# Optimization experiments

Hardware: AMD Instinct MI355X
Metric: run time of the kernel (lower is better)

## Reference

```python
import jax, jax.numpy as jnp
import numpy as np

NUM_HEADS = 8

def setup_inputs() -> dict:
    key = jax.random.key(0)
    k1, k2, k3 = jax.random.split(key, 3)
    B, N, C = 4, 4096, 512
    x = jax.random.normal(k1, (B, N, C), dtype=jnp.float32)
    w_qkv = jax.random.normal(k2, (C, 3 * C), dtype=jnp.float32) * (1.0 / np.sqrt(C))
    w_proj = jax.random.normal(k3, (C, C), dtype=jnp.float32) * (1.0 / np.sqrt(C))
    b_proj = jnp.zeros((C,), dtype=jnp.float32)
    return {"x": x, "w_qkv": w_qkv, "w_proj": w_proj, "b_proj": b_proj}

def reference(x, w_qkv, w_proj, b_proj):
    B, N, C = x.shape
    H = NUM_HEADS
    D = C // H
    # qkv projection (no bias), split into q, k, v of shape [B, H, N, D]
    qkv = (x @ w_qkv).reshape(B, N, 3, H, D)
    qkv = jnp.transpose(qkv, (2, 0, 3, 1, 4))
    q, k, v = qkv[0], qkv[1], qkv[2]
    # q: softmax over head_dim; k: elu(k)+1 then softmax over sequence dim
    q = jax.nn.softmax(q, axis=-1)
    k = jax.nn.softmax(jax.nn.elu(k) + 1.0, axis=-2)
    # linear attention: context = k^T @ v  -> [B, H, D, D]
    context = jnp.einsum('bhnd,bhne->bhde', k, v)
    # out = q @ context -> [B, H, N, D]
    out = jnp.einsum('bhnd,bhde->bhne', q, context)
    out = jnp.transpose(out, (0, 2, 1, 3)).reshape(B, N, C)
    # output projection (dropout with p=0.0 is identity)
    return out @ w_proj + b_proj
```

## Files before the change

kernel.cpp:

```cpp
#include <hip/hip_runtime.h>
#include <hip/hip_bf16.h>

typedef unsigned short u16;
typedef __attribute__((ext_vector_type(8))) short bhalf8;
typedef __attribute__((ext_vector_type(4))) float fx4;

struct __align__(8) US4 { u16 v[4]; };

__device__ __forceinline__ u16 f2bf(float x) {
  union { float f; unsigned int u; } c; c.f = x;
  unsigned int r = c.u + 0x7FFFu + ((c.u >> 16) & 1u);
  return (u16)(r >> 16);
}

__device__ __forceinline__ void gload16(const void* g, void* l) {
  __builtin_amdgcn_global_load_lds((const __attribute__((address_space(1))) void*)g,
                                   (__attribute__((address_space(3))) void*)l,
                                   16, 0, 0);
}

#define MFMA16(a, b, c) __builtin_amdgcn_mfma_f32_16x16x32_bf16((a), (b), (c), 0, 0, 0)

__global__ void k_conv(const float* __restrict__ in, u16* __restrict__ out, int n4) {
  int i = blockIdx.x * 256 + threadIdx.x;
  if (i < n4) {
    float4 v = ((const float4*)in)[i];
    US4 o;
    o.v[0] = f2bf(v.x); o.v[1] = f2bf(v.y); o.v[2] = f2bf(v.z); o.v[3] = f2bf(v.w);
    ((US4*)out)[i] = o;
  }
}

__global__ void k_transpose(const float* __restrict__ in, u16* __restrict__ out,
                            int R, int C, int rtiles, int remap) {
  __shared__ float tile[64][65];
  const int bx = blockIdx.x;
  const int rt = bx % rtiles, ct = bx / rtiles;
  const int r0 = rt * 64, c0 = ct * 64;
  const int t = threadIdx.x;
  #pragma unroll
  for (int i = 0; i < 16; ++i) {
    int e = i * 256 + t;
    int rr = e >> 6, cc = e & 63;
    tile[rr][cc] = in[(r0 + rr) * C + c0 + cc];
  }
  __syncthreads();
  #pragma unroll
  for (int i = 0; i < 16; ++i) {
    int e = i * 256 + t;
    int rr = e >> 6, cc = e & 63;
    int orow = c0 + rr;
    if (remap && orow >= 512) {
      int region = (orow - 512) >> 9;
      int within = (orow - 512) & 511;
      int h = within >> 6;
      orow = 512 + h * 128 + region * 64 + (within & 63);
    }
    out[orow * R + r0 + cc] = f2bf(tile[cc][rr]);
  }
}

__device__ __forceinline__ void gemm_core(const char* Ab, const char* Bb,
                                          char* As, char* Bs, fx4 acc[4][4]) {
  const int t = threadIdx.x;
  const int w = t >> 6, l = t & 63;
  const int wm = w >> 1, wn = w & 1;
  #pragma unroll 1
  for (int kt = 0; kt < 8; ++kt) {
    __syncthreads();
    const int kb = kt * 128;
    #pragma unroll
    for (int j = 0; j < 4; ++j) {
      int off = ((j * 4 + w) * 64 + l) * 16;
      int row = off >> 7;
      int colb = off & 127;
      int scol = colb ^ ((row & 7) << 4);
      gload16(Ab + row * 1024 + kb + scol, As + off);
      gload16(Bb + row * 1024 + kb + scol, Bs + off);
    }
    asm volatile("s_waitcnt vmcnt(0)" ::: "memory");
    __syncthreads();
    #pragma unroll
    for (int ks = 0; ks < 2; ++ks) {
      bhalf8 af[4], bfv[4];
      const int kbyte = ks * 64 + ((l >> 4) * 16);
      #pragma unroll
      for (int f = 0; f < 4; ++f) {
        int ra = wm * 64 + f * 16 + (l & 15);
        af[f] = *(const bhalf8*)(As + ra * 128 + (kbyte ^ ((ra & 7) << 4)));
        int rb = wn * 64 + f * 16 + (l & 15);
        bfv[f] = *(const bhalf8*)(Bs + rb * 128 + (kbyte ^ ((rb & 7) << 4)));
      }
      #pragma unroll
      for (int fm = 0; fm < 4; ++fm)
        #pragma unroll
        for (int fn = 0; fn < 4; ++fn)
          acc[fm][fn] = MFMA16(af[fm], bfv[fn], acc[fm][fn]);
    }
  }
}

__global__ __launch_bounds__(256, 2)
void k_qkv_gemm(const char* __restrict__ xb, const char* __restrict__ wqT,
                u16* __restrict__ qhat, float* __restrict__ ctx_part,
                float* __restrict__ z_part) {
  __shared__ __align__(16) char lds[32768];
  const int bx = blockIdx.x;
  const int tM = bx & 127, tN = bx >> 7;
  fx4 acc[4][4];
  const fx4 z4 = {0.f, 0.f, 0.f, 0.f};
  #pragma unroll
  for (int i = 0; i < 4; ++i)
    #pragma unroll
    for (int j = 0; j < 4; ++j) acc[i][j] = z4;

  gemm_core(xb + tM * 131072, wqT + tN * 131072, lds, lds + 16384, acc);

  const int t = threadIdx.x, w = t >> 6, l = t & 63;
  const int wm = w >> 1, wn = w & 1;
  const int m0 = tM * 128 + wm * 64;
  const int c0 = tN * 128 + wn * 64;

  if (tN < 4) {
    #pragma unroll
    for (int fm = 0; fm < 4; ++fm) {
      #pragma unroll
      for (int fn = 0; fn < 4; ++fn)
        #pragma unroll
        for (int r = 0; r < 4; ++r)
          acc[fm][fn][r] = __expf(acc[fm][fn][r]);
      fx4 s = acc[fm][0] + acc[fm][1] + acc[fm][2] + acc[fm][3];
      fx4 inv;
      #pragma unroll
      for (int r = 0; r < 4; ++r) {
        float sv = s[r];
        sv += __shfl_xor(sv, 1, 64);
        sv += __shfl_xor(sv, 2, 64);
        sv += __shfl_xor(sv, 4, 64);
        sv += __shfl_xor(sv, 8, 64);
        inv[r] = 1.0f / sv;
      }
      #pragma unroll
      for (int fn = 0; fn < 4; ++fn)
        #pragma unroll
        for (int r = 0; r < 4; ++r) {
          int m = m0 + fm * 16 + ((l >> 4) * 4) + r;
          int c = c0 + fn * 16 + (l & 15);
          qhat[m * 512 + c] = f2bf(acc[fm][fn][r] * inv[r]);
        }
    }
  } else {
    const int h = tN - 4;
    const int b = tM >> 5;
    const int mt = tM & 31;
    const int bh = b * 8 + h;
    char* ktb = lds;
    char* vtb = lds + 16384;
    __syncthreads();
    {
      char* dstb = (wn == 0) ? ktb : vtb;
      const bool isK = (wn == 0);
      #pragma unroll
      for (int fm = 0; fm < 4; ++fm)
        #pragma unroll
        for (int fn = 0; fn < 4; ++fn) {
          int d = fn * 16 + (l & 15);
          int n0 = wm * 64 + fm * 16 + ((l >> 4) * 4);
          US4 p;
          #pragma unroll
          for (int r = 0; r < 4; ++r) {
            float v = acc[fm][fn][r];
            if (isK) { float tt = v > 0.f ? v + 1.f : __expf(v); v = __expf(tt); }
            p.v[r] = f2bf(v);
          }
          *(US4*)(dstb + d * 256 + ((2 * n0) ^ ((d & 7) << 4))) = p;
        }
    }
    __syncthreads();
    fx4 cacc[4]; fx4 zacc = z4;
    #pragma unroll
    for (int fn = 0; fn < 4; ++fn) cacc[fn] = z4;
    bhalf8 ones;
    #pragma unroll
    for (int i = 0; i < 8; ++i) ones[i] = (short)0x3F80;
    #pragma unroll
    for (int kk = 0; kk < 4; ++kk) {
      int nbyte = kk * 64 + ((l >> 4) * 16);
      int d = w * 16 + (l & 15);
      bhalf8 a = *(const bhalf8*)(ktb + d * 256 + (nbyte ^ ((d & 7) << 4)));
      #pragma unroll
      for (int fn = 0; fn < 4; ++fn) {
        int e = fn * 16 + (l & 15);
        bhalf8 bv = *(const bhalf8*)(vtb + e * 256 + (nbyte ^ ((e & 7) << 4)));
        cacc[fn] = MFMA16(a, bv, cacc[fn]);
      }
      zacc = MFMA16(a, ones, zacc);
    }
    float* cp = ctx_part + (bh * 32 + mt) * 4096;
    #pragma unroll
    for (int fn = 0; fn < 4; ++fn)
      #pragma unroll
      for (int r = 0; r < 4; ++r) {
        int d = w * 16 + ((l >> 4) * 4) + r;
        int e = fn * 16 + (l & 15);
        cp[d * 64 + e] = cacc[fn][r];
      }
    if ((l & 15) == 0) {
      #pragma unroll
      for (int r = 0; r < 4; ++r)
        z_part[(bh * 32 + mt) * 64 + w * 16 + ((l >> 4) * 4) + r] = zacc[r];
    }
  }
}

__global__ __launch_bounds__(256)
void k_reduce(const float* __restrict__ ctx_part, float* __restrict__ ctx32) {
  const int bx = blockIdx.x;
  const int bh = bx >> 4;
  const int idx = (bx & 15) * 256 + threadIdx.x;
  float s = 0.f;
  #pragma unroll
  for (int mt = 0; mt < 32; ++mt)
    s += ctx_part[(bh * 32 + mt) * 4096 + idx];
  ctx32[bh * 4096 + idx] = s;
}

__global__ __launch_bounds__(256, 1)
void k_w2(const float* __restrict__ ctx32, const float* __restrict__ z_part,
          const u16* __restrict__ wpT, u16* __restrict__ W2T) {
  const int bh = blockIdx.x;
  const int b = bh >> 3, h = bh & 7;
  __shared__ float zinv[64];
  __shared__ __align__(16) u16 alds[64][72];
  const int t = threadIdx.x;
  if (t < 64) {
    float zs = 0.f;
    #pragma unroll
    for (int mt = 0; mt < 32; ++mt) zs += z_part[(bh * 32 + mt) * 64 + t];
    zinv[t] = 1.0f / zs;
  }
  __syncthreads();
  #pragma unroll
  for (int i = 0; i < 16; ++i) {
    int idx = i * 256 + t;
    int d = idx >> 6, e = idx & 63;
    alds[d][e] = f2bf(ctx32[bh * 4096 + idx] * zinv[d]);
  }
  __syncthreads();
  const int w = t >> 6, l = t & 63;
  fx4 acc[4][8];
  const fx4 z4 = {0.f, 0.f, 0.f, 0.f};
  #pragma unroll
  for (int i = 0; i < 4; ++i)
    #pragma unroll
    for (int j = 0; j < 8; ++j) acc[i][j] = z4;
  #pragma unroll
  for (int ks = 0; ks < 2; ++ks) {
    bhalf8 af[4];
    #pragma unroll
    for (int fm = 0; fm < 4; ++fm) {
      int row = fm * 16 + (l & 15);
      af[fm] = *(const bhalf8*)((const char*)alds + row * 144 + ks * 64 + ((l >> 4) * 16));
    }
    #pragma unroll
    for (int fn = 0; fn < 8; ++fn) {
      int c = w * 128 + fn * 16 + (l & 15);
      bhalf8 bv = *(const bhalf8*)(wpT + c * 512 + h * 64 + ks * 32 + ((l >> 4) * 8));
      #pragma unroll
      for (int fm = 0; fm < 4; ++fm)
        acc[fm][fn] = MFMA16(af[fm], bv, acc[fm][fn]);
    }
  }
  #pragma unroll
  for (int fm = 0; fm < 4; ++fm)
    #pragma unroll
    for (int fn = 0; fn < 8; ++fn) {
      int c = w * 128 + fn * 16 + (l & 15);
      int d0 = fm * 16 + ((l >> 4) * 4);
      US4 p;
      #pragma unroll
      for (int r = 0; r < 4; ++r) p.v[r] = f2bf(acc[fm][fn][r]);
      *(US4*)(W2T + (b * 512 + c) * 512 + h * 64 + d0) = p;
    }
}

__global__ __launch_bounds__(256, 2)
void k_out_gemm(const char* __restrict__ qhat, const char* __restrict__ W2T,
                const float* __restrict__ bproj, float* __restrict__ outp) {
  __shared__ __align__(16) char lds[32768];
  const int bx = blockIdx.x;
  const int tM = bx & 127, tN = bx >> 7;
  const int b = tM >> 5;
  fx4 acc[4][4];
  const fx4 z4 = {0.f, 0.f, 0.f, 0.f};
  #pragma unroll
  for (int i = 0; i < 4; ++i)
    #pragma unroll
    for (int j = 0; j < 4; ++j) acc[i][j] = z4;

  gemm_core(qhat + tM * 131072, W2T + b * 524288 + tN * 131072, lds, lds + 16384, acc);

  const int t = threadIdx.x, w = t >> 6, l = t & 63;
  const int wm = w >> 1, wn = w & 1;
  const int m0 = tM * 128 + wm * 64;
  const int c0 = tN * 128 + wn * 64;
  #pragma unroll
  for (int fm = 0; fm < 4; ++fm)
    #pragma unroll
    for (int fn = 0; fn < 4; ++fn) {
      int c = c0 + fn * 16 + (l & 15);
      float bp = bproj[c];
      #pragma unroll
      for (int r = 0; r < 4; ++r) {
        int m = m0 + fm * 16 + ((l >> 4) * 4) + r;
        outp[m * 512 + c] = acc[fm][fn][r] + bp;
      }
    }
}

extern "C" void kernel_launch(void* const* d_in, const int* in_sizes, int n_in,
                              void* d_out, int out_size, void* d_ws, size_t ws_size,
                              hipStream_t stream) {
  (void)in_sizes; (void)n_in; (void)out_size;
  const float* x     = (const float*)d_in[0];
  const float* wqkv  = (const float*)d_in[1];
  const float* wproj = (const float*)d_in[2];
  const float* bproj = (const float*)d_in[3];
  float* outp = (float*)d_out;
  char* ws = (char*)d_ws;

  char* xb   = ws;
  char* wqT  = ws + 16777216;
  char* wpT  = ws + 18350080;
  char* qhat = ws + 18874368;
  char* ctxp = ws + 35651584;
  char* zp   = ws + 52428800;
  char* ctx32= ws + 52690944;
  char* w2t  = ws + 53215232;
  if (ws_size < 55312384) return;

  k_conv<<<8192, 256, 0, stream>>>(x, (u16*)xb, 2097152);
  k_transpose<<<192, 256, 0, stream>>>(wqkv, (u16*)wqT, 512, 1536, 8, 1);
  k_transpose<<<64, 256, 0, stream>>>(wproj, (u16*)wpT, 512, 512, 8, 0);
  k_qkv_gemm<<<1536, 256, 0, stream>>>(xb, wqT, (u16*)qhat, (float*)ctxp, (float*)zp);
  k_reduce<<<512, 256, 0, stream>>>((const float*)ctxp, (float*)ctx32);
  k_w2<<<32, 256, 0, stream>>>((const float*)ctx32, (const float*)zp, (const u16*)wpT, (u16*)w2t);
  k_out_gemm<<<512, 256, 0, stream>>>(qhat, w2t, bproj, outp);
}
```

Baseline: 83.79 us.

## Triple-buffer async LDS loads with 256x128 tiles in both GEMM kernels

Replaces the single-buffered GEMM core with a triple-buffered pipeline. Global-to-LDS loads for tile kt+2 are issued while tile kt is computed, and a partial vmcnt wait replaces the full drain plus two barriers per step. Blocks grow to 512 threads covering 256x128 output tiles, with MFMA priority raised through setprio. The K/V context epilogue and the partial-sum reductions are adjusted to 16 partials instead of 32. The 144 KB of LDS per block limits residency to one block per CU, and the output GEMM now launches only 256 blocks.

```diff
diff --git a/kernel.cpp b/kernel.cpp
--- a/kernel.cpp
+++ b/kernel.cpp
@@ -20,6 +20,7 @@
 }
 
 #define MFMA16(a, b, c) __builtin_amdgcn_mfma_f32_16x16x32_bf16((a), (b), (c), 0, 0, 0)
+#define FENCE() asm volatile("" ::: "memory")
 
 __global__ void k_conv(const float* __restrict__ in, u16* __restrict__ out, int n4) {
   int i = blockIdx.x * 256 + threadIdx.x;
@@ -60,26 +61,52 @@
   }
 }
 
-__device__ __forceinline__ void gemm_core(const char* Ab, const char* Bb,
-                                          char* As, char* Bs, fx4 acc[4][4]) {
+__device__ __forceinline__ void gemm_core2(const char* Ab, const char* Bb,
+                                           char* lds, fx4 acc[4][4]) {
   const int t = threadIdx.x;
   const int w = t >> 6, l = t & 63;
   const int wm = w >> 1, wn = w & 1;
+
+  #define STAGE_A(buf, kt, j) do {                                   \
+    int off_ = ((j) * 512 + t) * 16;                                 \
+    int row_ = off_ >> 7;                                            \
+    int scol_ = (off_ & 127) ^ ((row_ & 7) << 4);                    \
+    gload16(Ab + row_ * 1024 + (kt) * 128 + scol_,                   \
+            lds + (buf) * 49152 + off_);                             \
+  } while (0)
+  #define STAGE_B(buf, kt, j) do {                                   \
+    int off_ = ((j) * 512 + t) * 16;                                 \
+    int row_ = off_ >> 7;                                            \
+    int scol_ = (off_ & 127) ^ ((row_ & 7) << 4);                    \
+    gload16(Bb + row_ * 1024 + (kt) * 128 + scol_,                   \
+            lds + (buf) * 49152 + 32768 + off_);                     \
+  } while (0)
+
+  #pragma unroll
+  for (int j = 0; j < 4; ++j) STAGE_A(0, 0, j);
+  #pragma unroll
+  for (int j = 0; j < 2; ++j) STAGE_B(0, 0, j);
+  #pragma unroll
+  for (int j = 0; j < 4; ++j) STAGE_A(1, 1, j);
+  #pragma unroll
+  for (int j = 0; j < 2; ++j) STAGE_B(1, 1, j);
+  asm volatile("s_waitcnt vmcnt(6)" ::: "memory");
+  __builtin_amdgcn_s_barrier();
+  FENCE();
+  __builtin_amdgcn_sched_barrier(0);
+
   #pragma unroll 1
   for (int kt = 0; kt < 8; ++kt) {
-    __syncthreads();
-    const int kb = kt * 128;
-    #pragma unroll
-    for (int j = 0; j < 4; ++j) {
-      int off = ((j * 4 + w) * 64 + l) * 16;
-      int row = off >> 7;
-      int colb = off & 127;
-      int scol = colb ^ ((row & 7) << 4);
-      gload16(Ab + row * 1024 + kb + scol, As + off);
-      gload16(Bb + row * 1024 + kb + scol, Bs + off);
-    }
-    asm volatile("s_waitcnt vmcnt(0)" ::: "memory");
-    __syncthreads();
+    const int p = kt % 3;
+    const char* As = lds + p * 49152;
+    const char* Bs = As + 32768;
+    if (kt < 6) {
+      const int np = (kt + 2) % 3;
+      STAGE_A(np, kt + 2, 0); STAGE_A(np, kt + 2, 1);
+      STAGE_B(np, kt + 2, 0);
+      STAGE_A(np, kt + 2, 2); STAGE_A(np, kt + 2, 3);
+      STAGE_B(np, kt + 2, 1);
+    }
     #pragma unroll
     for (int ks = 0; ks < 2; ++ks) {
       bhalf8 af[4], bfv[4];
@@ -91,22 +118,31 @@
         int rb = wn * 64 + f * 16 + (l & 15);
         bfv[f] = *(const bhalf8*)(Bs + rb * 128 + (kbyte ^ ((rb & 7) << 4)));
       }
+      __builtin_amdgcn_s_setprio(1);
       #pragma unroll
       for (int fm = 0; fm < 4; ++fm)
         #pragma unroll
         for (int fn = 0; fn < 4; ++fn)
           acc[fm][fn] = MFMA16(af[fm], bfv[fn], acc[fm][fn]);
-    }
-  }
-}
-
-__global__ __launch_bounds__(256, 2)
+      __builtin_amdgcn_s_setprio(0);
+    }
+    if (kt < 6) asm volatile("s_waitcnt vmcnt(6)" ::: "memory");
+    else        asm volatile("s_waitcnt vmcnt(0)" ::: "memory");
+    __builtin_amdgcn_s_barrier();
+    FENCE();
+    __builtin_amdgcn_sched_barrier(0);
+  }
+  #undef STAGE_A
+  #undef STAGE_B
+}
+
+__global__ __launch_bounds__(512, 2)
 void k_qkv_gemm(const char* __restrict__ xb, const char* __restrict__ wqT,
                 u16* __restrict__ qhat, float* __restrict__ ctx_part,
                 float* __restrict__ z_part) {
-  __shared__ __align__(16) char lds[32768];
+  __shared__ __align__(16) char lds[147456];
   const int bx = blockIdx.x;
-  const int tM = bx & 127, tN = bx >> 7;
+  const int tM = bx & 63, tN = bx >> 6;
   fx4 acc[4][4];
   const fx4 z4 = {0.f, 0.f, 0.f, 0.f};
   #pragma unroll
@@ -114,11 +150,11 @@
     #pragma unroll
     for (int j = 0; j < 4; ++j) acc[i][j] = z4;
 
-  gemm_core(xb + tM * 131072, wqT + tN * 131072, lds, lds + 16384, acc);
+  gemm_core2(xb + tM * 262144, wqT + tN * 131072, lds, acc);
 
   const int t = threadIdx.x, w = t >> 6, l = t & 63;
   const int wm = w >> 1, wn = w & 1;
-  const int m0 = tM * 128 + wm * 64;
+  const int m0 = tM * 256 + wm * 64;
   const int c0 = tN * 128 + wn * 64;
 
   if (tN < 4) {
@@ -151,11 +187,11 @@
     }
   } else {
     const int h = tN - 4;
-    const int b = tM >> 5;
-    const int mt = tM & 31;
+    const int b = tM >> 4;
+    const int mt = tM & 15;
     const int bh = b * 8 + h;
     char* ktb = lds;
-    char* vtb = lds + 16384;
+    char* vtb = lds + 32768;
     __syncthreads();
     {
       char* dstb = (wn == 0) ? ktb : vtb;
@@ -173,42 +209,41 @@
             if (isK) { float tt = v > 0.f ? v + 1.f : __expf(v); v = __expf(tt); }
             p.v[r] = f2bf(v);
           }
-          *(US4*)(dstb + d * 256 + ((2 * n0) ^ ((d & 7) << 4))) = p;
+          *(US4*)(dstb + d * 512 + ((2 * n0) ^ ((d & 7) << 4))) = p;
         }
     }
     __syncthreads();
-    fx4 cacc[4]; fx4 zacc = z4;
-    #pragma unroll
-    for (int fn = 0; fn < 4; ++fn) cacc[fn] = z4;
+    fx4 cacc[2]; fx4 zacc = z4;
+    cacc[0] = z4; cacc[1] = z4;
     bhalf8 ones;
     #pragma unroll
     for (int i = 0; i < 8; ++i) ones[i] = (short)0x3F80;
     #pragma unroll
-    for (int kk = 0; kk < 4; ++kk) {
+    for (int kk = 0; kk < 8; ++kk) {
       int nbyte = kk * 64 + ((l >> 4) * 16);
-      int d = w * 16 + (l & 15);
-      bhalf8 a = *(const bhalf8*)(ktb + d * 256 + (nbyte ^ ((d & 7) << 4)));
-      #pragma unroll
-      for (int fn = 0; fn < 4; ++fn) {
-        int e = fn * 16 + (l & 15);
-        bhalf8 bv = *(const bhalf8*)(vtb + e * 256 + (nbyte ^ ((e & 7) << 4)));
+      int d = wm * 16 + (l & 15);
+      bhalf8 a = *(const bhalf8*)(ktb + d * 512 + (nbyte ^ ((d & 7) << 4)));
+      #pragma unroll
+      for (int fn = 0; fn < 2; ++fn) {
+        int e = wn * 32 + fn * 16 + (l & 15);
+        bhalf8 bv = *(const bhalf8*)(vtb + e * 512 + (nbyte ^ ((e & 7) << 4)));
         cacc[fn] = MFMA16(a, bv, cacc[fn]);
       }
-      zacc = MFMA16(a, ones, zacc);
-    }
-    float* cp = ctx_part + (bh * 32 + mt) * 4096;
-    #pragma unroll
-    for (int fn = 0; fn < 4; ++fn)
+      if (wn == 0) zacc = MFMA16(a, ones, zacc);
+    }
+    float* cp = ctx_part + (bh * 16 + mt) * 4096;
+    #pragma unroll
+    for (int fn = 0; fn < 2; ++fn)
       #pragma unroll
       for (int r = 0; r < 4; ++r) {
-        int d = w * 16 + ((l >> 4) * 4) + r;
-        int e = fn * 16 + (l & 15);
+        int d = wm * 16 + ((l >> 4) * 4) + r;
+        int e = wn * 32 + fn * 16 + (l & 15);
         cp[d * 64 + e] = cacc[fn][r];
       }
-    if ((l & 15) == 0) {
+    if (wn == 0 && (l & 15) == 0) {
       #pragma unroll
       for (int r = 0; r < 4; ++r)
-        z_part[(bh * 32 + mt) * 64 + w * 16 + ((l >> 4) * 4) + r] = zacc[r];
+        z_part[(bh * 16 + mt) * 64 + wm * 16 + ((l >> 4) * 4) + r] = zacc[r];
     }
   }
 }
@@ -220,8 +255,8 @@
   const int idx = (bx & 15) * 256 + threadIdx.x;
   float s = 0.f;
   #pragma unroll
-  for (int mt = 0; mt < 32; ++mt)
-    s += ctx_part[(bh * 32 + mt) * 4096 + idx];
+  for (int mt = 0; mt < 16; ++mt)
+    s += ctx_part[(bh * 16 + mt) * 4096 + idx];
   ctx32[bh * 4096 + idx] = s;
 }
 
@@ -236,7 +271,7 @@
   if (t < 64) {
     float zs = 0.f;
     #pragma unroll
-    for (int mt = 0; mt < 32; ++mt) zs += z_part[(bh * 32 + mt) * 64 + t];
+    for (int mt = 0; mt < 16; ++mt) zs += z_part[(bh * 16 + mt) * 64 + t];
     zinv[t] = 1.0f / zs;
   }
   __syncthreads();
@@ -284,13 +319,13 @@
     }
 }
 
-__global__ __launch_bounds__(256, 2)
+__global__ __launch_bounds__(512, 2)
 void k_out_gemm(const char* __restrict__ qhat, const char* __restrict__ W2T,
                 const float* __restrict__ bproj, float* __restrict__ outp) {
-  __shared__ __align__(16) char lds[32768];
+  __shared__ __align__(16) char lds[147456];
   const int bx = blockIdx.x;
-  const int tM = bx & 127, tN = bx >> 7;
-  const int b = tM >> 5;
+  const int tM = bx & 63, tN = bx >> 6;
+  const int b = tM >> 4;
   fx4 acc[4][4];
   const fx4 z4 = {0.f, 0.f, 0.f, 0.f};
   #pragma unroll
@@ -298,11 +333,11 @@
     #pragma unroll
     for (int j = 0; j < 4; ++j) acc[i][j] = z4;
 
-  gemm_core(qhat + tM * 131072, W2T + b * 524288 + tN * 131072, lds, lds + 16384, acc);
+  gemm_core2(qhat + tM * 262144, W2T + b * 524288 + tN * 131072, lds, acc);
 
   const int t = threadIdx.x, w = t >> 6, l = t & 63;
   const int wm = w >> 1, wn = w & 1;
-  const int m0 = tM * 128 + wm * 64;
+  const int m0 = tM * 256 + wm * 64;
   const int c0 = tN * 128 + wn * 64;
   #pragma unroll
   for (int fm = 0; fm < 4; ++fm)
@@ -334,16 +369,16 @@
   char* wpT  = ws + 18350080;
   char* qhat = ws + 18874368;
   char* ctxp = ws + 35651584;
-  char* zp   = ws + 52428800;
-  char* ctx32= ws + 52690944;
-  char* w2t  = ws + 53215232;
-  if (ws_size < 55312384) return;
+  char* zp   = ws + 44040192;
+  char* ctx32= ws + 44171264;
+  char* w2t  = ws + 44695552;
+  if (ws_size < 46792704) return;
 
   k_conv<<<8192, 256, 0, stream>>>(x, (u16*)xb, 2097152);
   k_transpose<<<192, 256, 0, stream>>>(wqkv, (u16*)wqT, 512, 1536, 8, 1);
   k_transpose<<<64, 256, 0, stream>>>(wproj, (u16*)wpT, 512, 512, 8, 0);
-  k_qkv_gemm<<<1536, 256, 0, stream>>>(xb, wqT, (u16*)qhat, (float*)ctxp, (float*)zp);
+  k_qkv_gemm<<<768, 512, 0, stream>>>(xb, wqT, (u16*)qhat, (float*)ctxp, (float*)zp);
   k_reduce<<<512, 256, 0, stream>>>((const float*)ctxp, (float*)ctx32);
   k_w2<<<32, 256, 0, stream>>>((const float*)ctx32, (const float*)zp, (const u16*)wpT, (u16*)w2t);
-  k_out_gemm<<<512, 256, 0, stream>>>(qhat, w2t, bproj, outp);
-}
+  k_out_gemm<<<256, 512, 0, stream>>>(qhat, w2t, bproj, outp);
+}
```

After: 87.23 us. 1.04x slower.

## Fuse fp32-to-bf16 conversion of x into QKV GEMM load and swizzle block order

Applied to the files above, without the earlier changes.

Drops the separate conversion kernel that wrote a bf16 copy of x. The QKV GEMM now reads fp32 x directly into registers, converts it with the hardware bf16 conversion, and stores it swizzled into LDS, which removes one kernel launch and a full write and read of the bf16 activation buffer. Both GEMMs also remap block IDs so that consecutive blocks are spread across what appear to be XCD groups, aiming at better L2 reuse. In exchange, A-tile loads now go through registers without overlap, which may leave the GEMM more latency-bound.

```diff
diff --git a/kernel.cpp b/kernel.cpp
--- a/kernel.cpp
+++ b/kernel.cpp
@@ -6,6 +6,7 @@
 typedef __attribute__((ext_vector_type(4))) float fx4;
 
 struct __align__(8) US4 { u16 v[4]; };
+struct __align__(16) US8 { u16 v[8]; };
 
 __device__ __forceinline__ u16 f2bf(float x) {
   union { float f; unsigned int u; } c; c.f = x;
@@ -13,6 +14,12 @@
   return (u16)(r >> 16);
 }
 
+__device__ __forceinline__ u16 f2bf_hw(float x) {
+  union { __hip_bfloat16 h; u16 u; } c;
+  c.h = __float2bfloat16(x);
+  return c.u;
+}
+
 __device__ __forceinline__ void gload16(const void* g, void* l) {
   __builtin_amdgcn_global_load_lds((const __attribute__((address_space(1))) void*)g,
                                    (__attribute__((address_space(3))) void*)l,
@@ -20,16 +27,6 @@
 }
 
 #define MFMA16(a, b, c) __builtin_amdgcn_mfma_f32_16x16x32_bf16((a), (b), (c), 0, 0, 0)
-
-__global__ void k_conv(const float* __restrict__ in, u16* __restrict__ out, int n4) {
-  int i = blockIdx.x * 256 + threadIdx.x;
-  if (i < n4) {
-    float4 v = ((const float4*)in)[i];
-    US4 o;
-    o.v[0] = f2bf(v.x); o.v[1] = f2bf(v.y); o.v[2] = f2bf(v.z); o.v[3] = f2bf(v.w);
-    ((US4*)out)[i] = o;
-  }
-}
 
 __global__ void k_transpose(const float* __restrict__ in, u16* __restrict__ out,
                             int R, int C, int rtiles, int remap) {
@@ -60,6 +57,61 @@
   }
 }
 
+__device__ __forceinline__ void gemm_core_f32A(const float* __restrict__ Ax,
+                                               const char* __restrict__ Bb,
+                                               char* As, char* Bs, fx4 acc[4][4]) {
+  const int t = threadIdx.x;
+  const int w = t >> 6, l = t & 63;
+  const int wm = w >> 1, wn = w & 1;
+  const int arow = t >> 1, ah = t & 1;
+  const float4* asrc = (const float4*)(Ax + arow * 512 + ah * 32);
+  char* adst = As + arow * 128;
+  const int aswz = (arow & 7) << 4;
+  #pragma unroll 1
+  for (int kt = 0; kt < 8; ++kt) {
+    __syncthreads();
+    float4 av[8];
+    #pragma unroll
+    for (int q = 0; q < 8; ++q) av[q] = asrc[kt * 16 + q];
+    const int kb = kt * 128;
+    #pragma unroll
+    for (int j = 0; j < 4; ++j) {
+      int off = ((j * 4 + w) * 64 + l) * 16;
+      int row = off >> 7;
+      int scol = (off & 127) ^ ((row & 7) << 4);
+      gload16(Bb + row * 1024 + kb + scol, Bs + off);
+    }
+    #pragma unroll
+    for (int q = 0; q < 4; ++q) {
+      US8 p;
+      p.v[0] = f2bf_hw(av[2 * q].x);     p.v[1] = f2bf_hw(av[2 * q].y);
+      p.v[2] = f2bf_hw(av[2 * q].z);     p.v[3] = f2bf_hw(av[2 * q].w);
+      p.v[4] = f2bf_hw(av[2 * q + 1].x); p.v[5] = f2bf_hw(av[2 * q + 1].y);
+      p.v[6] = f2bf_hw(av[2 * q + 1].z); p.v[7] = f2bf_hw(av[2 * q + 1].w);
+      *(US8*)(adst + ((ah * 64 + q * 16) ^ aswz)) = p;
+    }
+    asm volatile("s_waitcnt vmcnt(0)" ::: "memory");
+    __syncthreads();
+    #pragma unroll
+    for (int ks = 0; ks < 2; ++ks) {
+      bhalf8 af[4], bfv[4];
+      const int kbyte = ks * 64 + ((l >> 4) * 16);
+      #pragma unroll
+      for (int f = 0; f < 4; ++f) {
+        int ra = wm * 64 + f * 16 + (l & 15);
+        af[f] = *(const bhalf8*)(As + ra * 128 + (kbyte ^ ((ra & 7) << 4)));
+        int rb = wn * 64 + f * 16 + (l & 15);
+        bfv[f] = *(const bhalf8*)(Bs + rb * 128 + (kbyte ^ ((rb & 7) << 4)));
+      }
+      #pragma unroll
+      for (int fm = 0; fm < 4; ++fm)
+        #pragma unroll
+        for (int fn = 0; fn < 4; ++fn)
+          acc[fm][fn] = MFMA16(af[fm], bfv[fn], acc[fm][fn]);
+    }
+  }
+}
+
 __device__ __forceinline__ void gemm_core(const char* Ab, const char* Bb,
                                           char* As, char* Bs, fx4 acc[4][4]) {
   const int t = threadIdx.x;
@@ -101,12 +153,13 @@
 }
 
 __global__ __launch_bounds__(256, 2)
-void k_qkv_gemm(const char* __restrict__ xb, const char* __restrict__ wqT,
+void k_qkv_gemm(const float* __restrict__ x, const char* __restrict__ wqT,
                 u16* __restrict__ qhat, float* __restrict__ ctx_part,
                 float* __restrict__ z_part) {
   __shared__ __align__(16) char lds[32768];
-  const int bx = blockIdx.x;
-  const int tM = bx & 127, tN = bx >> 7;
+  const int bid = blockIdx.x;
+  const int nb = (bid & 7) * 192 + (bid >> 3);
+  const int tM = nb & 127, tN = nb >> 7;
   fx4 acc[4][4];
   const fx4 z4 = {0.f, 0.f, 0.f, 0.f};
   #pragma unroll
@@ -114,7 +167,7 @@
     #pragma unroll
     for (int j = 0; j < 4; ++j) acc[i][j] = z4;
 
-  gemm_core(xb + tM * 131072, wqT + tN * 131072, lds, lds + 16384, acc);
+  gemm_core_f32A(x + tM * 65536, wqT + tN * 131072, lds, lds + 16384, acc);
 
   const int t = threadIdx.x, w = t >> 6, l = t & 63;
   const int wm = w >> 1, wn = w & 1;
@@ -288,8 +341,9 @@
 void k_out_gemm(const char* __restrict__ qhat, const char* __restrict__ W2T,
                 const float* __restrict__ bproj, float* __restrict__ outp) {
   __shared__ __align__(16) char lds[32768];
-  const int bx = blockIdx.x;
-  const int tM = bx & 127, tN = bx >> 7;
+  const int bid = blockIdx.x;
+  const int nb = (bid & 7) * 64 + (bid >> 3);
+  const int tM = nb & 127, tN = nb >> 7;
   const int b = tM >> 5;
   fx4 acc[4][4];
   const fx4 z4 = {0.f, 0.f, 0.f, 0.f};
@@ -329,20 +383,18 @@
   float* outp = (float*)d_out;
   char* ws = (char*)d_ws;
 
-  char* xb   = ws;
-  char* wqT  = ws + 16777216;
-  char* wpT  = ws + 18350080;
-  char* qhat = ws + 18874368;
-  char* ctxp = ws + 35651584;
-  char* zp   = ws + 52428800;
-  char* ctx32= ws + 52690944;
-  char* w2t  = ws + 53215232;
-  if (ws_size < 55312384) return;
-
-  k_conv<<<8192, 256, 0, stream>>>(x, (u16*)xb, 2097152);
+  char* wqT  = ws;
+  char* wpT  = ws + 1572864;
+  char* qhat = ws + 2097152;
+  char* ctxp = ws + 18874368;
+  char* zp   = ws + 35651584;
+  char* ctx32= ws + 35913728;
+  char* w2t  = ws + 36438016;
+  if (ws_size < 38535168) return;
+
   k_transpose<<<192, 256, 0, stream>>>(wqkv, (u16*)wqT, 512, 1536, 8, 1);
   k_transpose<<<64, 256, 0, stream>>>(wproj, (u16*)wpT, 512, 512, 8, 0);
-  k_qkv_gemm<<<1536, 256, 0, stream>>>(xb, wqT, (u16*)qhat, (float*)ctxp, (float*)zp);
+  k_qkv_gemm<<<1536, 256, 0, stream>>>(x, wqT, (u16*)qhat, (float*)ctxp, (float*)zp);
   k_reduce<<<512, 256, 0, stream>>>((const float*)ctxp, (float*)ctx32);
   k_w2<<<32, 256, 0, stream>>>((const float*)ctx32, (const float*)zp, (const u16*)wpT, (u16*)w2t);
   k_out_gemm<<<512, 256, 0, stream>>>(qhat, w2t, bproj, outp);
```

Measured after the change: 114.3 us. 1.36x slower.

## Merge prep kernels, store context partials in bf16, vectorize reduction

Applied to the files above, without the earlier changes.

Folds the x conversion and both weight transposes into a single prep launch, cutting two kernel launches. The per-tile context partial sums are now stored as bf16 instead of fp32, halving that intermediate's write and read traffic. The reduction kernel reads four bf16 values per thread and writes float4, using fewer blocks. Rounding the partials to bf16 adds precision loss before the sum.

```diff
diff --git a/kernel.cpp b/kernel.cpp
--- a/kernel.cpp
+++ b/kernel.cpp
@@ -13,6 +13,11 @@
   return (u16)(r >> 16);
 }
 
+__device__ __forceinline__ float bf2f(u16 v) {
+  union { unsigned int u; float f; } c; c.u = ((unsigned int)v) << 16;
+  return c.f;
+}
+
 __device__ __forceinline__ void gload16(const void* g, void* l) {
   __builtin_amdgcn_global_load_lds((const __attribute__((address_space(1))) void*)g,
                                    (__attribute__((address_space(3))) void*)l,
@@ -21,23 +26,26 @@
 
 #define MFMA16(a, b, c) __builtin_amdgcn_mfma_f32_16x16x32_bf16((a), (b), (c), 0, 0, 0)
 
-__global__ void k_conv(const float* __restrict__ in, u16* __restrict__ out, int n4) {
-  int i = blockIdx.x * 256 + threadIdx.x;
-  if (i < n4) {
-    float4 v = ((const float4*)in)[i];
+__global__ __launch_bounds__(256)
+void k_prep(const float* __restrict__ x, u16* __restrict__ xb,
+            const float* __restrict__ wqkv, u16* __restrict__ wqT,
+            const float* __restrict__ wproj, u16* __restrict__ wpT) {
+  __shared__ float tile[64][65];
+  const int bx = blockIdx.x;
+  const int t = threadIdx.x;
+  if (bx < 8192) {
+    int i = bx * 256 + t;
+    float4 v = ((const float4*)x)[i];
     US4 o;
     o.v[0] = f2bf(v.x); o.v[1] = f2bf(v.y); o.v[2] = f2bf(v.z); o.v[3] = f2bf(v.w);
-    ((US4*)out)[i] = o;
-  }
-}
-
-__global__ void k_transpose(const float* __restrict__ in, u16* __restrict__ out,
-                            int R, int C, int rtiles, int remap) {
-  __shared__ float tile[64][65];
-  const int bx = blockIdx.x;
-  const int rt = bx % rtiles, ct = bx / rtiles;
+    ((US4*)xb)[i] = o;
+    return;
+  }
+  const float* in; u16* out; int C, remap, bx2;
+  if (bx < 8384) { in = wqkv; out = wqT; C = 1536; remap = 1; bx2 = bx - 8192; }
+  else           { in = wproj; out = wpT; C = 512;  remap = 0; bx2 = bx - 8384; }
+  const int rt = bx2 & 7, ct = bx2 >> 3;
   const int r0 = rt * 64, c0 = ct * 64;
-  const int t = threadIdx.x;
   #pragma unroll
   for (int i = 0; i < 16; ++i) {
     int e = i * 256 + t;
@@ -56,7 +64,7 @@
       int h = within >> 6;
       orow = 512 + h * 128 + region * 64 + (within & 63);
     }
-    out[orow * R + r0 + cc] = f2bf(tile[cc][rr]);
+    out[orow * 512 + r0 + cc] = f2bf(tile[cc][rr]);
   }
 }
 
@@ -102,7 +110,7 @@
 
 __global__ __launch_bounds__(256, 2)
 void k_qkv_gemm(const char* __restrict__ xb, const char* __restrict__ wqT,
-                u16* __restrict__ qhat, float* __restrict__ ctx_part,
+                u16* __restrict__ qhat, u16* __restrict__ ctx_part,
                 float* __restrict__ z_part) {
   __shared__ __align__(16) char lds[32768];
   const int bx = blockIdx.x;
@@ -196,14 +204,14 @@
       }
       zacc = MFMA16(a, ones, zacc);
     }
-    float* cp = ctx_part + (bh * 32 + mt) * 4096;
+    u16* cp = ctx_part + (bh * 32 + mt) * 4096;
     #pragma unroll
     for (int fn = 0; fn < 4; ++fn)
       #pragma unroll
       for (int r = 0; r < 4; ++r) {
         int d = w * 16 + ((l >> 4) * 4) + r;
         int e = fn * 16 + (l & 15);
-        cp[d * 64 + e] = cacc[fn][r];
+        cp[d * 64 + e] = f2bf(cacc[fn][r]);
       }
     if ((l & 15) == 0) {
       #pragma unroll
@@ -214,15 +222,18 @@
 }
 
 __global__ __launch_bounds__(256)
-void k_reduce(const float* __restrict__ ctx_part, float* __restrict__ ctx32) {
-  const int bx = blockIdx.x;
-  const int bh = bx >> 4;
-  const int idx = (bx & 15) * 256 + threadIdx.x;
-  float s = 0.f;
-  #pragma unroll
-  for (int mt = 0; mt < 32; ++mt)
-    s += ctx_part[(bh * 32 + mt) * 4096 + idx];
-  ctx32[bh * 4096 + idx] = s;
+void k_reduce(const u16* __restrict__ ctx_part, float* __restrict__ ctx32) {
+  const int bid = blockIdx.x;
+  const int bh = bid >> 2;
+  const int idx0 = (bid & 3) * 1024 + threadIdx.x * 4;
+  float s0 = 0.f, s1 = 0.f, s2 = 0.f, s3 = 0.f;
+  #pragma unroll
+  for (int mt = 0; mt < 32; ++mt) {
+    US4 p = *(const US4*)(ctx_part + (bh * 32 + mt) * 4096 + idx0);
+    s0 += bf2f(p.v[0]); s1 += bf2f(p.v[1]); s2 += bf2f(p.v[2]); s3 += bf2f(p.v[3]);
+  }
+  float4 o; o.x = s0; o.y = s1; o.z = s2; o.w = s3;
+  *(float4*)(ctx32 + bh * 4096 + idx0) = o;
 }
 
 __global__ __launch_bounds__(256, 1)
@@ -334,16 +345,14 @@
   char* wpT  = ws + 18350080;
   char* qhat = ws + 18874368;
   char* ctxp = ws + 35651584;
-  char* zp   = ws + 52428800;
-  char* ctx32= ws + 52690944;
-  char* w2t  = ws + 53215232;
-  if (ws_size < 55312384) return;
-
-  k_conv<<<8192, 256, 0, stream>>>(x, (u16*)xb, 2097152);
-  k_transpose<<<192, 256, 0, stream>>>(wqkv, (u16*)wqT, 512, 1536, 8, 1);
-  k_transpose<<<64, 256, 0, stream>>>(wproj, (u16*)wpT, 512, 512, 8, 0);
-  k_qkv_gemm<<<1536, 256, 0, stream>>>(xb, wqT, (u16*)qhat, (float*)ctxp, (float*)zp);
-  k_reduce<<<512, 256, 0, stream>>>((const float*)ctxp, (float*)ctx32);
+  char* zp   = ws + 44040192;
+  char* ctx32= ws + 44302336;
+  char* w2t  = ws + 44826624;
+  if (ws_size < 46923776) return;
+
+  k_prep<<<8448, 256, 0, stream>>>(x, (u16*)xb, wqkv, (u16*)wqT, wproj, (u16*)wpT);
+  k_qkv_gemm<<<1536, 256, 0, stream>>>(xb, wqT, (u16*)qhat, (u16*)ctxp, (float*)zp);
+  k_reduce<<<128, 256, 0, stream>>>((const u16*)ctxp, (float*)ctx32);
   k_w2<<<32, 256, 0, stream>>>((const float*)ctx32, (const float*)zp, (const u16*)wpT, (u16*)w2t);
   k_out_gemm<<<512, 256, 0, stream>>>(qhat, w2t, bproj, outp);
 }
```

Result: faster. 79.48 us, median of 2 (-5.1%).
